# Kernel optimization log

Hardware: AMD Instinct MI355X
Metric: run time of the kernel (lower is better)

Reference implementation:

```python
import jax, jax.numpy as jnp
import numpy as np

ENC_HID = 512
DEC_HID = 1024
ATTN_DIM = 1024
ATTN_IN = ENC_HID * 2 + DEC_HID  # 2048
B, S = 32, 1024


def setup_inputs() -> dict:
    key = jax.random.key(0)
    k1, k2, k3, k4, k5 = jax.random.split(key, 5)
    decoder_hidden = jax.random.normal(k1, (B, DEC_HID), dtype=jnp.float32)
    encoder_outputs = jax.random.normal(k2, (B, S, 2 * ENC_HID), dtype=jnp.float32)
    # nn.Linear(attn_in, attn_dim): weight [attn_dim, attn_in], bias [attn_dim]
    lim = 1.0 / np.sqrt(ATTN_IN)
    W = jax.random.uniform(k3, (ATTN_IN, ATTN_DIM), jnp.float32, -lim, lim)
    b = jax.random.uniform(k4, (ATTN_DIM,), jnp.float32, -lim, lim)
    v = jax.random.uniform(k5, (ATTN_DIM,), jnp.float32, 0.0, 1.0)
    return {"decoder_hidden": decoder_hidden, "encoder_outputs": encoder_outputs,
            "W": W, "b": b, "v": v}


def reference(decoder_hidden, encoder_outputs, W, b, v):
    # Avoid materializing the repeat+concat: split the Linear weight into the
    # decoder-hidden block and the encoder-outputs block. Same math as
    # tanh(Linear(cat([dec_rep, enc], -1))).
    W_dec = W[:DEC_HID]          # [dec_hid, attn_dim]
    W_enc = W[DEC_HID:]          # [2*enc_hid, attn_dim]
    dec_proj = decoder_hidden @ W_dec + b                     # [B, A]
    enc_proj = jnp.einsum('bse,ea->bsa', encoder_outputs, W_enc)  # [B, S, A]
    energy = jnp.tanh(enc_proj + dec_proj[:, None, :])        # [B, S, A]
    attention = jnp.einsum('bsa,a->bs', energy, v)            # [B, S]
    return jax.nn.softmax(attention, axis=1)
```

## Files before the change

kernel.cpp:

```cpp
#include <hip/hip_runtime.h>
#include <stdint.h>

#define ENC2 1024
#define DECH 1024
#define ADIM 1024
#define BB   32
#define SS   1024

typedef _Float16 half_t;
typedef __attribute__((ext_vector_type(4))) _Float16 half4;
typedef __attribute__((ext_vector_type(8))) _Float16 half8;
typedef __attribute__((ext_vector_type(4))) float    f32x4;

__device__ __forceinline__ void dma16(const half_t* g, half_t* l) {
    __builtin_amdgcn_global_load_lds((const __attribute__((address_space(1))) void*)g,
                                     (__attribute__((address_space(3))) void*)l,
                                     16, 0, 0);
}

__global__ __launch_bounds__(512) void k_prep(const float* __restrict__ enc,
                                              const float* __restrict__ W,
                                              const float* __restrict__ dh,
                                              half_t* __restrict__ e16,
                                              half_t* __restrict__ Wt2,
                                              float* __restrict__ dpart) {
    __shared__ __align__(16) char smem[33792];
    const int bid = blockIdx.x;
    const int t = threadIdx.x;

    if (bid < 2048) {
        half_t (*Lt)[264] = (half_t (*)[264])smem;
        const int rblk = bid >> 2, cblk = bid & 3;
        const int r0 = rblk * 64, k0 = cblk * 256;
        #pragma unroll
        for (int i = 0; i < 8; i++) {
            int row = i * 8 + (t >> 6);
            int col = (t & 63) * 4;
            float4 vv = *(const float4*)&enc[(size_t)(r0 + row) * ENC2 + k0 + col];
            half4 h;
            h[0] = (half_t)vv.x; h[1] = (half_t)vv.y;
            h[2] = (half_t)vv.z; h[3] = (half_t)vv.w;
            *(half4*)&Lt[row][col] = h;
        }
        __syncthreads();
        const int mi = rblk >> 1, p = rblk & 1;
        const int ks0 = cblk * 8;
        #pragma unroll
        for (int j = 0; j < 4; j++) {
            int u = j * 512 + t;
            int pair = u >> 6, l = u & 63;
            int ksl = pair >> 2, quad = pair & 3;
            half8 h = *(const half8*)&Lt[l][ksl * 32 + quad * 8];
            size_t chunk = (size_t)(mi * 32 + ks0 + ksl) * 8 + quad * 2 + p;
            *(half8*)&e16[(chunk << 9) + l * 8];
            *(half8*)&e16[(chunk << 9) + l * 8] = h;
        }
    } else if (bid < 2176) {
        float (*tile)[257] = (float (*)[257])smem;
        const int blk = bid - 2048;
        const int nb = blk >> 5;
        const int ks = blk & 31;
        #pragma unroll
        for (int i = 0; i < 16; i++) {
            int idx = t + i * 512;
            int kr = idx >> 8, n = idx & 255;
            tile[kr][n] = W[(size_t)(DECH + ks * 32 + kr) * ADIM + nb * 256 + n];
        }
        __syncthreads();
        half_t* reg = Wt2 + ((size_t)(nb * 32 + ks) << 13);
        #pragma unroll
        for (int i = 0; i < 2; i++) {
            int cid = t + i * 512;
            int r = cid >> 2, pos = cid & 3;
            int c = pos ^ ((r >> 1) & 3);
            half8 h;
            #pragma unroll
            for (int e = 0; e < 8; e++) h[e] = (half_t)tile[c * 8 + e][r];
            *(half8*)(reg + r * 32 + pos * 8) = h;
        }
    } else {
        float (*red)[BB][64] = (float (*)[BB][64])smem;
        const int blk = bid - 2176;
        const int ct = blk & 15;
        const int kc = blk >> 4;
        if (t < 256) {
            const int col = ct * 64 + (t & 63);
            const int w = t >> 6;
            const int k0 = kc * 128 + w * 32;
            float wreg[32];
            #pragma unroll
            for (int kk = 0; kk < 32; kk++)
                wreg[kk] = W[(size_t)(k0 + kk) * ADIM + col];
            float s[BB];
            #pragma unroll
            for (int b = 0; b < BB; b++) s[b] = 0.f;
            #pragma unroll
            for (int kk = 0; kk < 32; kk++) {
                #pragma unroll
                for (int b = 0; b < BB; b++)
                    s[b] += dh[b * DECH + k0 + kk] * wreg[kk];
            }
            #pragma unroll
            for (int b = 0; b < BB; b++) red[w][b][t & 63] = s[b];
        }
        __syncthreads();
        if (t < 64) {
            for (int b = 0; b < BB; b++)
                dpart[((size_t)kc * BB + b) * ADIM + ct * 64 + t] =
                    red[0][b][t] + red[1][b][t] + red[2][b][t] + red[3][b][t];
        }
    }
}

#define BM 128
#define BN 256
#define BK 32

__global__ __launch_bounds__(512, 4) void k_main(const half_t* __restrict__ encA,
                                                 const half_t* __restrict__ Wt2,
                                                 const float* __restrict__ dpart,
                                                 const float* __restrict__ bias,
                                                 const float* __restrict__ v,
                                                 float* __restrict__ scores_part) {
    __shared__ half_t lsA[2][4096];
    __shared__ half_t lsB[2][8192];

    const int bid = blockIdx.x;
    const int mi = (bid >> 5) * 8 + (bid & 7);
    const int nb = (bid >> 3) & 3;
    const int m0 = mi * BM;
    const int t = threadIdx.x;
    const int w = t >> 6, L = t & 63;
    const int wm = w & 1, wn = w >> 1;
    const int lane15 = L & 15, quad = L >> 4;

    const half_t* Abase = encA + ((size_t)mi << 17);
    const half_t* Bbase = Wt2 + ((size_t)(nb * 32) << 13);

    f32x4 acc[4][4];
    #pragma unroll
    for (int i = 0; i < 4; i++)
        #pragma unroll
        for (int j = 0; j < 4; j++) acc[i][j] = (f32x4)0.f;

    auto dmaA = [&](int ks, int pb) {
        dma16(Abase + (((size_t)ks * 8 + w) << 9) + L * 8, &lsA[pb][w * 512]);
    };
    auto dmaB = [&](int ks, int pb) {
        #pragma unroll
        for (int jj = 0; jj < 2; jj++) {
            int j = 2 * w + jj;
            dma16(Bbase + ((size_t)ks << 13) + j * 512 + L * 8,
                  &lsB[pb][j * 512]);
        }
    };

    dmaA(0, 0);
    dmaB(0, 0);
    __syncthreads();

    for (int ks = 0; ks < ENC2 / BK; ks++) {
        const int cur = ks & 1;
        if (ks < ENC2 / BK - 1) {
            dmaA(ks + 1, cur ^ 1);
            dmaB(ks + 1, cur ^ 1);
        }
        half8 af[4], bf[4];
        #pragma unroll
        for (int sm = 0; sm < 4; sm++)
            af[sm] = *(const half8*)&lsA[cur][quad * 1024 +
                                              (wm * 64 + sm * 16 + lane15) * 8];
        #pragma unroll
        for (int sn = 0; sn < 4; sn++) {
            int r = wn * 64 + sn * 16 + lane15;
            int pos = quad ^ ((r >> 1) & 3);
            bf[sn] = *(const half8*)&lsB[cur][r * 32 + pos * 8];
        }
        #pragma unroll
        for (int sm = 0; sm < 4; sm++)
            #pragma unroll
            for (int sn = 0; sn < 4; sn++)
                acc[sm][sn] = __builtin_amdgcn_mfma_f32_16x16x32_f16(
                    af[sm], bf[sn], acc[sm][sn], 0, 0, 0);
        __syncthreads();
    }

    const int batch = mi >> 3;
    float vv[4], dp[4];
    #pragma unroll
    for (int sn = 0; sn < 4; sn++) {
        int ng = nb * BN + wn * 64 + sn * 16 + lane15;
        vv[sn] = v[ng];
        float s = bias[ng];
        #pragma unroll
        for (int kc = 0; kc < 8; kc++)
            s += dpart[((size_t)kc * BB + batch) * ADIM + ng];
        dp[sn] = s;
    }

    float* redL = (float*)&lsA[0][0];
    #pragma unroll
    for (int sm = 0; sm < 4; sm++) {
        #pragma unroll
        for (int rr = 0; rr < 4; rr++) {
            float s = 0.f;
            #pragma unroll
            for (int sn = 0; sn < 4; sn++) {
                float x = acc[sm][sn][rr] + dp[sn];
                float e  = __builtin_amdgcn_exp2f(x * 2.8853900817779268f);
                float th = 1.f - 2.f * __builtin_amdgcn_rcpf(e + 1.f);
                s += th * vv[sn];
            }
            s += __shfl_xor(s, 1, 64);
            s += __shfl_xor(s, 2, 64);
            s += __shfl_xor(s, 4, 64);
            s += __shfl_xor(s, 8, 64);
            if (lane15 == 0) {
                int mlocal = wm * 64 + sm * 16 + quad * 4 + rr;
                redL[wn * 128 + mlocal] = s;
            }
        }
    }
    __syncthreads();
    if (t < 128) {
        float s = redL[t] + redL[128 + t] + redL[256 + t] + redL[384 + t];
        scores_part[((size_t)nb << 15) + m0 + t] = s;
    }
}

__global__ __launch_bounds__(256) void k_softmax(const float* __restrict__ sp,
                                                 float* __restrict__ out) {
    __shared__ float red[8];
    const int b = blockIdx.x, t = threadIdx.x;
    float x[4];
    #pragma unroll
    for (int i = 0; i < 4; i++) {
        size_t idx = (size_t)b * SS + t + i * 256;
        x[i] = sp[idx] + sp[(1u << 15) + idx] + sp[(2u << 15) + idx] +
               sp[(3u << 15) + idx];
    }
    float mx = fmaxf(fmaxf(x[0], x[1]), fmaxf(x[2], x[3]));
    #pragma unroll
    for (int d = 1; d < 64; d <<= 1) mx = fmaxf(mx, __shfl_xor(mx, d, 64));
    if ((t & 63) == 0) red[t >> 6] = mx;
    __syncthreads();
    mx = fmaxf(fmaxf(red[0], red[1]), fmaxf(red[2], red[3]));
    float e[4], s = 0.f;
    #pragma unroll
    for (int i = 0; i < 4; i++) {
        e[i] = __builtin_amdgcn_exp2f((x[i] - mx) * 1.4426950408889634f);
        s += e[i];
    }
    #pragma unroll
    for (int d = 1; d < 64; d <<= 1) s += __shfl_xor(s, d, 64);
    if ((t & 63) == 0) red[4 + (t >> 6)] = s;
    __syncthreads();
    s = red[4] + red[5] + red[6] + red[7];
    float inv = 1.f / s;
    #pragma unroll
    for (int i = 0; i < 4; i++) out[(size_t)b * SS + t + i * 256] = e[i] * inv;
}

__global__ __launch_bounds__(256) void k_wt_f(const float* __restrict__ W,
                                              half_t* __restrict__ Wt2) {
    __shared__ float tile[32][257];
    const int nb = blockIdx.x >> 5;
    const int ks = blockIdx.x & 31;
    const int t = threadIdx.x;
    #pragma unroll
    for (int i = 0; i < 32; i++) {
        int idx = t + i * 256;
        int kr = idx >> 8, n = idx & 255;
        tile[kr][n] = W[(size_t)(DECH + ks * 32 + kr) * ADIM + nb * 256 + n];
    }
    __syncthreads();
    half_t* reg = Wt2 + ((size_t)(nb * 32 + ks) << 13);
    #pragma unroll
    for (int i = 0; i < 4; i++) {
        int cid = t + i * 256;
        int r = cid >> 2, pos = cid & 3;
        int c = pos ^ ((r >> 1) & 3);
        half8 h;
        #pragma unroll
        for (int e = 0; e < 8; e++) h[e] = (half_t)tile[c * 8 + e][r];
        *(half8*)(reg + r * 32 + pos * 8) = h;
    }
}

__global__ __launch_bounds__(256) void k_dp1_f(const float* __restrict__ dh,
                                               const float* __restrict__ W,
                                               float* __restrict__ part) {
    __shared__ float red[4][BB][64];
    const int t = threadIdx.x;
    const int ct = blockIdx.x & 15;
    const int kc = blockIdx.x >> 4;
    const int col = ct * 64 + (t & 63);
    const int w = t >> 6;
    const int k0 = kc * 128 + w * 32;
    float wreg[32];
    #pragma unroll
    for (int kk = 0; kk < 32; kk++)
        wreg[kk] = W[(size_t)(k0 + kk) * ADIM + col];
    float s[BB];
    #pragma unroll
    for (int b = 0; b < BB; b++) s[b] = 0.f;
    #pragma unroll
    for (int kk = 0; kk < 32; kk++) {
        #pragma unroll
        for (int b = 0; b < BB; b++)
            s[b] += dh[b * DECH + k0 + kk] * wreg[kk];
    }
    #pragma unroll
    for (int b = 0; b < BB; b++) red[w][b][t & 63] = s[b];
    __syncthreads();
    if (t < 64) {
        for (int b = 0; b < BB; b++)
            part[((size_t)kc * BB + b) * ADIM + ct * 64 + t] =
                red[0][b][t] + red[1][b][t] + red[2][b][t] + red[3][b][t];
    }
}

__global__ __launch_bounds__(256) void k_dp2_f(const float* __restrict__ part,
                                               const float* __restrict__ bias,
                                               float* __restrict__ decp) {
    const int i = blockIdx.x * 256 + threadIdx.x;
    float s = bias[i & (ADIM - 1)];
    #pragma unroll
    for (int kc = 0; kc < 8; kc++)
        s += part[(size_t)kc * BB * ADIM + i];
    decp[i] = s;
}

#define LDA 40
__global__ __launch_bounds__(512, 4) void k_main_reg(const float* __restrict__ enc,
                                                     const half_t* __restrict__ Wt2,
                                                     const float* __restrict__ decp,
                                                     const float* __restrict__ v,
                                                     float* __restrict__ scores_part) {
    __shared__ half_t lsA[2][BM][LDA];
    __shared__ half_t lsB[2][BN * BK];

    const int bid = blockIdx.x;
    const int mi = (bid >> 5) * 8 + (bid & 7);
    const int nb = (bid >> 3) & 3;
    const int m0 = mi * BM;
    const int t = threadIdx.x;
    const int w = t >> 6, L = t & 63;
    const int wm = w & 1, wn = w >> 1;
    const int lane15 = L & 15, quad = L >> 4;

    const int arow = t & 127;
    const int akc  = (t >> 7) * 8;
    const float* Aptr = enc + (size_t)(m0 + arow) * ENC2 + akc;
    const half_t* Bbase = Wt2 + ((size_t)(nb * 32) << 13);

    f32x4 acc[4][4];
    #pragma unroll
    for (int i = 0; i < 4; i++)
        #pragma unroll
        for (int j = 0; j < 4; j++) acc[i][j] = (f32x4)0.f;

    float4 ra0, ra1;
    auto loadA = [&](int ks) {
        const float* p = Aptr + ks * BK;
        ra0 = *(const float4*)p;
        ra1 = *(const float4*)(p + 4);
    };
    auto writeA = [&](int pb) {
        half8 ha;
        ha[0] = (half_t)ra0.x; ha[1] = (half_t)ra0.y;
        ha[2] = (half_t)ra0.z; ha[3] = (half_t)ra0.w;
        ha[4] = (half_t)ra1.x; ha[5] = (half_t)ra1.y;
        ha[6] = (half_t)ra1.z; ha[7] = (half_t)ra1.w;
        *(half8*)&lsA[pb][arow][akc] = ha;
    };
    auto dmaB = [&](int ks, int pb) {
        #pragma unroll
        for (int jj = 0; jj < 2; jj++) {
            int j = 2 * w + jj;
            dma16(Bbase + ((size_t)ks << 13) + j * 512 + L * 8,
                  &lsB[pb][j * 512]);
        }
    };

    dmaB(0, 0);
    loadA(0);
    writeA(0);
    loadA(1);
    __syncthreads();

    for (int ks = 0; ks < ENC2 / BK; ks++) {
        const int cur = ks & 1;
        if (ks < ENC2 / BK - 1) {
            dmaB(ks + 1, cur ^ 1);
            writeA(cur ^ 1);
            if (ks < ENC2 / BK - 2) loadA(ks + 2);
        }
        half8 af[4], bf[4];
        #pragma unroll
        for (int sm = 0; sm < 4; sm++)
            af[sm] = *(const half8*)&lsA[cur][wm * 64 + sm * 16 + lane15][quad * 8];
        #pragma unroll
        for (int sn = 0; sn < 4; sn++) {
            int r = wn * 64 + sn * 16 + lane15;
            int pos = quad ^ ((r >> 1) & 3);
            bf[sn] = *(const half8*)&lsB[cur][r * 32 + pos * 8];
        }
        #pragma unroll
        for (int sm = 0; sm < 4; sm++)
            #pragma unroll
            for (int sn = 0; sn < 4; sn++)
                acc[sm][sn] = __builtin_amdgcn_mfma_f32_16x16x32_f16(
                    af[sm], bf[sn], acc[sm][sn], 0, 0, 0);
        __syncthreads();
    }

    const int batch = mi >> 3;
    float vv[4], dp[4];
    #pragma unroll
    for (int sn = 0; sn < 4; sn++) {
        int ng = nb * BN + wn * 64 + sn * 16 + lane15;
        vv[sn] = v[ng];
        dp[sn] = decp[(size_t)batch * ADIM + ng];
    }

    float* redL = (float*)&lsA[0][0][0];
    #pragma unroll
    for (int sm = 0; sm < 4; sm++) {
        #pragma unroll
        for (int rr = 0; rr < 4; rr++) {
            float s = 0.f;
            #pragma unroll
            for (int sn = 0; sn < 4; sn++) {
                float x = acc[sm][sn][rr] + dp[sn];
                float e  = __builtin_amdgcn_exp2f(x * 2.8853900817779268f);
                float th = 1.f - 2.f * __builtin_amdgcn_rcpf(e + 1.f);
                s += th * vv[sn];
            }
            s += __shfl_xor(s, 1, 64);
            s += __shfl_xor(s, 2, 64);
            s += __shfl_xor(s, 4, 64);
            s += __shfl_xor(s, 8, 64);
            if (lane15 == 0) {
                int mlocal = wm * 64 + sm * 16 + quad * 4 + rr;
                redL[wn * 128 + mlocal] = s;
            }
        }
    }
    __syncthreads();
    if (t < 128) {
        float s = redL[t] + redL[128 + t] + redL[256 + t] + redL[384 + t];
        scores_part[((size_t)nb << 15) + m0 + t] = s;
    }
}

extern "C" void kernel_launch(void* const* d_in, const int* in_sizes, int n_in,
                              void* d_out, int out_size, void* d_ws, size_t ws_size,
                              hipStream_t stream) {
    const float* dh   = (const float*)d_in[0];
    const float* enc  = (const float*)d_in[1];
    const float* W    = (const float*)d_in[2];
    const float* bias = (const float*)d_in[3];
    const float* v    = (const float*)d_in[4];
    float* out = (float*)d_out;

    char* ws = (char*)d_ws;
    const size_t E16_BYTES = (size_t)BB * SS * ENC2 * sizeof(half_t);
    const size_t NEED = (4u << 20) + E16_BYTES;

    if (ws_size >= NEED) {
        half_t* Wt2   = (half_t*)ws;
        float*  dpart = (float*)(ws + (2u << 20));
        float*  spart = (float*)(ws + (3u << 20));
        half_t* e16   = (half_t*)(ws + (4u << 20));

        k_prep   <<<2304, 512, 0, stream>>>(enc, W, dh, e16, Wt2, dpart);
        k_main   <<<1024, 512, 0, stream>>>(e16, Wt2, dpart, bias, v, spart);
        k_softmax<<<32, 256, 0, stream>>>(spart, out);
    } else {
        half_t* Wt2   = (half_t*)ws;
        float*  decp  = (float*)(ws + 2u * 1024 * 1024);
        float*  spart = (float*)(ws + 2u * 1024 * 1024 + 128 * 1024);
        float*  dpart = (float*)(ws + 2u * 1024 * 1024 + 640 * 1024);

        k_wt_f   <<<128, 256, 0, stream>>>(W, Wt2);
        k_dp1_f  <<<128, 256, 0, stream>>>(dh, W, dpart);
        k_dp2_f  <<<128, 256, 0, stream>>>(dpart, bias, decp);
        k_main_reg<<<1024, 512, 0, stream>>>(enc, Wt2, decp, v, spart);
        k_softmax<<<32, 256, 0, stream>>>(spart, out);
    }
}
```

Baseline: 283.5 us.

## Triple-buffer GEMM LDS staging with explicit vmcnt waits and raw barriers

Moves the main GEMM loop from double to triple buffering of the A and B tiles in LDS, issuing DMA loads two k-steps ahead. Explicit s_waitcnt vmcnt counts replace full __syncthreads so only the oldest stage's loads are awaited, and sched barriers pin the instruction order. It also drops a stray dead load expression in the prep kernel. LDS use per block grows by half, which may reduce the number of blocks resident per CU under launch_bounds(512,4).

```diff
diff --git a/kernel.cpp b/kernel.cpp
--- a/kernel.cpp
+++ b/kernel.cpp
@@ -17,6 +17,13 @@
                                      (__attribute__((address_space(3))) void*)l,
                                      16, 0, 0);
 }
+
+#define VM6()   asm volatile("s_waitcnt vmcnt(6)" ::: "memory")
+#define VM3()   asm volatile("s_waitcnt vmcnt(3)" ::: "memory")
+#define VM0()   asm volatile("s_waitcnt vmcnt(0)" ::: "memory")
+#define LGKM0() asm volatile("s_waitcnt lgkmcnt(0)" ::: "memory")
+#define SCHED0() __builtin_amdgcn_sched_barrier(0)
+#define RBAR()  __builtin_amdgcn_s_barrier()
 
 __global__ __launch_bounds__(512) void k_prep(const float* __restrict__ enc,
                                               const float* __restrict__ W,
@@ -52,7 +59,6 @@
             int ksl = pair >> 2, quad = pair & 3;
             half8 h = *(const half8*)&Lt[l][ksl * 32 + quad * 8];
             size_t chunk = (size_t)(mi * 32 + ks0 + ksl) * 8 + quad * 2 + p;
-            *(half8*)&e16[(chunk << 9) + l * 8];
             *(half8*)&e16[(chunk << 9) + l * 8] = h;
         }
     } else if (bid < 2176) {
@@ -122,8 +128,8 @@
                                                  const float* __restrict__ bias,
                                                  const float* __restrict__ v,
                                                  float* __restrict__ scores_part) {
-    __shared__ half_t lsA[2][4096];
-    __shared__ half_t lsB[2][8192];
+    __shared__ half_t lsA[3][4096];
+    __shared__ half_t lsB[3][8192];
 
     const int bid = blockIdx.x;
     const int mi = (bid >> 5) * 8 + (bid & 7);
@@ -143,10 +149,8 @@
         #pragma unroll
         for (int j = 0; j < 4; j++) acc[i][j] = (f32x4)0.f;
 
-    auto dmaA = [&](int ks, int pb) {
+    auto stage = [&](int ks, int pb) {
         dma16(Abase + (((size_t)ks * 8 + w) << 9) + L * 8, &lsA[pb][w * 512]);
-    };
-    auto dmaB = [&](int ks, int pb) {
         #pragma unroll
         for (int jj = 0; jj < 2; jj++) {
             int j = 2 * w + jj;
@@ -155,16 +159,23 @@
         }
     };
 
-    dmaA(0, 0);
-    dmaB(0, 0);
-    __syncthreads();
-
+    stage(0, 0);
+    stage(1, 1);
+
+    int cur = 0;
     for (int ks = 0; ks < ENC2 / BK; ks++) {
-        const int cur = ks & 1;
-        if (ks < ENC2 / BK - 1) {
-            dmaA(ks + 1, cur ^ 1);
-            dmaB(ks + 1, cur ^ 1);
-        }
+        const int nxt = (cur == 0) ? 2 : cur - 1;
+        if (ks < ENC2 / BK - 2) {
+            stage(ks + 2, nxt);
+            VM6();
+        } else if (ks == ENC2 / BK - 2) {
+            VM3();
+        } else {
+            VM0();
+        }
+        RBAR();
+        SCHED0();
+
         half8 af[4], bf[4];
         #pragma unroll
         for (int sm = 0; sm < 4; sm++)
@@ -176,13 +187,16 @@
             int pos = quad ^ ((r >> 1) & 3);
             bf[sn] = *(const half8*)&lsB[cur][r * 32 + pos * 8];
         }
+        LGKM0();
+        SCHED0();
         #pragma unroll
         for (int sm = 0; sm < 4; sm++)
             #pragma unroll
             for (int sn = 0; sn < 4; sn++)
                 acc[sm][sn] = __builtin_amdgcn_mfma_f32_16x16x32_f16(
                     af[sm], bf[sn], acc[sm][sn], 0, 0, 0);
-        __syncthreads();
+        RBAR();
+        cur = (cur == 2) ? 0 : cur + 1;
     }
 
     const int batch = mi >> 3;
```

Measured after the change: 281.3 us. About the same (-0.8%).
